# Optimization experiments

Hardware: AMD Instinct MI355X
Metric: run time of the kernel (lower is better)

The kernel has to match this reference:

```python
import jax, jax.numpy as jnp
import numpy as np

SEQ = 4096
D_MODEL = 2048


def setup_inputs() -> dict:
    key = jax.random.key(0)
    k1, k2, k3, k4 = jax.random.split(key, 4)
    scale = 1.0 / np.sqrt(D_MODEL)
    token_encodings = jax.random.normal(k1, (SEQ, D_MODEL), dtype=jnp.float32)
    W_q = jax.random.normal(k2, (D_MODEL, D_MODEL), dtype=jnp.float32) * scale
    W_k = jax.random.normal(k3, (D_MODEL, D_MODEL), dtype=jnp.float32) * scale
    W_v = jax.random.normal(k4, (D_MODEL, D_MODEL), dtype=jnp.float32) * scale
    # causal mask: True where attention is disallowed (strictly upper triangular),
    # mirroring `mask = mask == 0` applied to a lower-triangular ones matrix.
    mask = jnp.triu(jnp.ones((SEQ, SEQ), dtype=bool), k=1)
    return {"token_encodings": token_encodings, "W_q": W_q, "W_k": W_k,
            "W_v": W_v, "mask": mask}


def reference(token_encodings, W_q, W_k, W_v, mask):
    # nn.Linear(bias=False): y = x @ W.T
    q = token_encodings @ W_q.T  # [S, D]
    k = token_encodings @ W_k.T  # [S, D]
    v = token_encodings @ W_v.T  # [S, D]
    sims = q @ k.T               # [S, S]
    scaled = sims / jnp.asarray(np.sqrt(D_MODEL), dtype=sims.dtype)
    scaled = jnp.where(mask, jnp.asarray(-1e9, dtype=scaled.dtype), scaled)
    attn = jax.nn.softmax(scaled, axis=1)
    return attn @ v              # [S, D]
```

## Files before the change

### kernel.cpp

```cpp
#include <hip/hip_runtime.h>
#include <hip/hip_bf16.h>

typedef unsigned short u16;
typedef __attribute__((ext_vector_type(8))) short short8;
typedef __attribute__((ext_vector_type(4))) float f32x4;
typedef __attribute__((ext_vector_type(4))) unsigned short u16x4;

#define SEQL 4096
#define DMOD 2048

__device__ __forceinline__ u16 f2bf(float x) {
    unsigned int u = __float_as_uint(x);
    u += 0x7FFF + ((u >> 16) & 1);
    return (u16)(u >> 16);
}

__device__ __forceinline__ void async_copy16(const void* g, void* s) {
    __builtin_amdgcn_global_load_lds(
        (const __attribute__((address_space(1))) unsigned int*)g,
        (__attribute__((address_space(3))) unsigned int*)s,
        16, 0, 0);
}

__global__ __launch_bounds__(256)
void cast_all(const float* __restrict__ X,  const float* __restrict__ Wq,
              const float* __restrict__ Wk, const float* __restrict__ Wv,
              u16* __restrict__ Xb,  u16* __restrict__ Wqb,
              u16* __restrict__ Wkb, u16* __restrict__ Wvb)
{
    const int b = blockIdx.x;
    const float* in; u16* out; int i;
    if (b < 8192) { in = X; out = Xb; i = b * 256 + threadIdx.x; }
    else {
        const int w  = (b - 8192) >> 12;
        const int lb = (b - 8192) & 4095;
        i = lb * 256 + threadIdx.x;
        in  = w == 0 ? Wq  : w == 1 ? Wk  : Wv;
        out = w == 0 ? Wqb : w == 1 ? Wkb : Wvb;
    }
    float4 v = ((const float4*)in)[i];
    u16x4 r;
    r[0] = f2bf(v.x); r[1] = f2bf(v.y); r[2] = f2bf(v.z); r[3] = f2bf(v.w);
    ((u16x4*)out)[i] = r;
}

__global__ __launch_bounds__(256)
void gemm_qkv64(const u16* __restrict__ A,
                const u16* __restrict__ B0, const u16* __restrict__ B1, const u16* __restrict__ B2,
                u16* __restrict__ C0, u16* __restrict__ C1, u16* __restrict__ C2)
{
    const int K = DMOD, N = DMOD;
    const int bid = blockIdx.x;
    const int e = bid & 7, idx = bid >> 3;
    const int br = idx / 6;
    const int bcAll = e * 6 + idx % 6;
    const int which = bcAll >> 4;
    const int rowBase = br * 128, colBase = (bcAll & 15) * 128;
    const u16* B = which == 0 ? B0 : which == 1 ? B1 : B2;
    u16*       C = which == 0 ? C0 : which == 1 ? C1 : C2;

    __shared__ __align__(16) u16 As[2][128 * 64];
    __shared__ __align__(16) u16 Bs[2][128 * 64];

    const int tid = threadIdx.x;
    const int wid = tid >> 6, lane = tid & 63;
    const int wr = wid >> 1, wc = wid & 1;
    const int q = lane >> 4, l15 = lane & 15;

    const int nkt = K >> 6;
    const u16* Ag = A + (size_t)rowBase * K;
    const u16* Bg = B + (size_t)colBase * K;
    const int srow = lane >> 3;
    const int scel = ((lane & 7) * 8) ^ (srow << 3);

    f32x4 acc[4][4] = {};

    auto stage = [&](int buf, int kt) {
        const int k0 = kt * 64;
        #pragma unroll
        for (int r = 0; r < 4; ++r) {
            const int rowl = wid * 32 + r * 8;
            async_copy16(Ag + (size_t)(rowl + srow) * K + k0 + scel, &As[buf][rowl * 64]);
            async_copy16(Bg + (size_t)(rowl + srow) * K + k0 + scel, &Bs[buf][rowl * 64]);
        }
    };

    stage(0, 0);
    asm volatile("s_waitcnt vmcnt(0)" ::: "memory");
    __builtin_amdgcn_s_barrier();
    for (int kt = 0; kt < nkt; ++kt) {
        const int cur = kt & 1;
        if (kt + 1 < nkt) stage(cur ^ 1, kt + 1);

        short8 af[2][4], bfr[2][4];
        #pragma unroll
        for (int ks = 0; ks < 2; ++ks) {
            #pragma unroll
            for (int m = 0; m < 4; ++m) {
                const int row = wr * 64 + m * 16 + l15;
                af[ks][m] = *(const short8*)&As[cur][row * 64 + ((ks * 32 + q * 8) ^ ((row & 7) << 3))];
            }
            #pragma unroll
            for (int n = 0; n < 4; ++n) {
                const int row = wc * 64 + n * 16 + l15;
                bfr[ks][n] = *(const short8*)&Bs[cur][row * 64 + ((ks * 32 + q * 8) ^ ((row & 7) << 3))];
            }
        }
        #pragma unroll
        for (int ks = 0; ks < 2; ++ks)
            #pragma unroll
            for (int m = 0; m < 4; ++m)
                #pragma unroll
                for (int n = 0; n < 4; ++n)
                    acc[m][n] = __builtin_amdgcn_mfma_f32_16x16x32_bf16(
                        af[ks][m], bfr[ks][n], acc[m][n], 0, 0, 0);

        asm volatile("s_waitcnt vmcnt(0)" ::: "memory");
        __builtin_amdgcn_s_barrier();
    }

    const int crow0 = rowBase + wr * 64 + (lane >> 4) * 4;
    const int ccol0 = colBase + wc * 64 + l15;
    #pragma unroll
    for (int m = 0; m < 4; ++m)
        #pragma unroll
        for (int n = 0; n < 4; ++n)
            #pragma unroll
            for (int r = 0; r < 4; ++r)
                C[(size_t)(crow0 + m * 16 + r) * N + (ccol0 + n * 16)] = f2bf(acc[m][n][r]);
}

template<int MODE>
__global__ __launch_bounds__(256)
void gemm_bt64(const u16* __restrict__ A, const u16* __restrict__ B,
               void* __restrict__ Cout, float* __restrict__ lsum,
               int N, int K, float scale)
{
    int br, bc;
    if (MODE == 2) {
        const int bid = blockIdx.x;
        const int e = bid & 7, idx = bid >> 3;
        const int g = idx >> 1;
        br = (g < 16) ? (2 * g) : (63 - 2 * g);
        bc = e * 2 + (idx & 1);
    } else {
        br = blockIdx.y; bc = blockIdx.x;
        if (bc > br) return;
    }
    const int rowBase = br * 128, colBase = bc * 128;

    __shared__ __align__(16) u16 As[2][128 * 64];
    __shared__ __align__(16) u16 Bs[2][128 * 64];

    const int tid = threadIdx.x;
    const int wid = tid >> 6, lane = tid & 63;
    const int wr = wid >> 1, wc = wid & 1;
    const int q = lane >> 4, l15 = lane & 15;

    int nkt = K >> 6;
    if (MODE == 2) { const int lim = br * 2 + 2; if (lim < nkt) nkt = lim; }

    const u16* Ag = A + (size_t)rowBase * K;
    const u16* Bg = B + (size_t)colBase * K;
    const int srow = lane >> 3;
    const int scel = ((lane & 7) * 8) ^ (srow << 3);

    f32x4 acc[4][4] = {};

    auto stage = [&](int buf, int kt) {
        const int k0 = kt * 64;
        #pragma unroll
        for (int r = 0; r < 4; ++r) {
            const int rowl = wid * 32 + r * 8;
            async_copy16(Ag + (size_t)(rowl + srow) * K + k0 + scel, &As[buf][rowl * 64]);
            async_copy16(Bg + (size_t)(rowl + srow) * K + k0 + scel, &Bs[buf][rowl * 64]);
        }
    };

    stage(0, 0);
    asm volatile("s_waitcnt vmcnt(0)" ::: "memory");
    __builtin_amdgcn_s_barrier();
    for (int kt = 0; kt < nkt; ++kt) {
        const int cur = kt & 1;
        if (kt + 1 < nkt) stage(cur ^ 1, kt + 1);

        short8 af[2][4], bfr[2][4];
        #pragma unroll
        for (int ks = 0; ks < 2; ++ks) {
            #pragma unroll
            for (int m = 0; m < 4; ++m) {
                const int row = wr * 64 + m * 16 + l15;
                af[ks][m] = *(const short8*)&As[cur][row * 64 + ((ks * 32 + q * 8) ^ ((row & 7) << 3))];
            }
            #pragma unroll
            for (int n = 0; n < 4; ++n) {
                const int row = wc * 64 + n * 16 + l15;
                bfr[ks][n] = *(const short8*)&Bs[cur][row * 64 + ((ks * 32 + q * 8) ^ ((row & 7) << 3))];
            }
        }
        #pragma unroll
        for (int ks = 0; ks < 2; ++ks)
            #pragma unroll
            for (int m = 0; m < 4; ++m)
                #pragma unroll
                for (int n = 0; n < 4; ++n)
                    acc[m][n] = __builtin_amdgcn_mfma_f32_16x16x32_bf16(
                        af[ks][m], bfr[ks][n], acc[m][n], 0, 0, 0);

        asm volatile("s_waitcnt vmcnt(0)" ::: "memory");
        __builtin_amdgcn_s_barrier();
    }

    const int crow0 = rowBase + wr * 64 + (lane >> 4) * 4;
    const int ccol0 = colBase + wc * 64 + l15;
    if (MODE == 1) {
        u16* E = (u16*)Cout;
        #pragma unroll
        for (int m = 0; m < 4; ++m)
            #pragma unroll
            for (int r = 0; r < 4; ++r) {
                const int row = crow0 + m * 16 + r;
                float rs = 0.f;
                #pragma unroll
                for (int n = 0; n < 4; ++n) {
                    const int col = ccol0 + n * 16;
                    float e = (col > row) ? 0.f : __expf(acc[m][n][r] * scale);
                    E[(size_t)row * N + col] = f2bf(e);
                    rs += e;
                }
                rs += __shfl_xor(rs, 1);
                rs += __shfl_xor(rs, 2);
                rs += __shfl_xor(rs, 4);
                rs += __shfl_xor(rs, 8);
                if (l15 == 0) atomicAdd(&lsum[row], rs);
            }
    } else {
        float* C = (float*)Cout;
        #pragma unroll
        for (int m = 0; m < 4; ++m)
            #pragma unroll
            for (int r = 0; r < 4; ++r) {
                const int row = crow0 + m * 16 + r;
                const float inv = 1.0f / lsum[row];
                #pragma unroll
                for (int n = 0; n < 4; ++n)
                    C[(size_t)row * N + (ccol0 + n * 16)] = acc[m][n][r] * inv;
            }
    }
}

__global__ __launch_bounds__(256)
void transpose_bf16(const u16* __restrict__ in, u16* __restrict__ out, int R, int C) {
    __shared__ u16 t[64][65];
    const int cb = blockIdx.x * 64, rb = blockIdx.y * 64;
    const int tx = threadIdx.x & 63, ty = threadIdx.x >> 6;
    #pragma unroll
    for (int i = 0; i < 16; ++i) {
        const int r = i * 4 + ty;
        t[r][tx] = in[(size_t)(rb + r) * C + cb + tx];
    }
    __syncthreads();
    #pragma unroll
    for (int i = 0; i < 16; ++i) {
        const int r = i * 4 + ty;
        out[(size_t)(cb + r) * R + rb + tx] = t[tx][r];
    }
}

extern "C" void kernel_launch(void* const* d_in, const int* in_sizes, int n_in,
                              void* d_out, int out_size, void* d_ws, size_t ws_size,
                              hipStream_t stream)
{
    const float* X  = (const float*)d_in[0];
    const float* Wq = (const float*)d_in[1];
    const float* Wk = (const float*)d_in[2];
    const float* Wv = (const float*)d_in[3];
    float* Out = (float*)d_out;

    char* ws = (char*)d_ws;
    const size_t MB = 1ull << 20;
    u16*   Xb   = (u16*)(ws + 0);
    u16*   Wqb  = (u16*)(ws + 16 * MB);
    u16*   Wkb  = (u16*)(ws + 24 * MB);
    u16*   Wvb  = (u16*)(ws + 32 * MB);
    u16*   E    = (u16*)(ws + 16 * MB);
    u16*   Qb   = (u16*)(ws + 48 * MB);
    u16*   Kb   = (u16*)(ws + 64 * MB);
    u16*   Vb   = (u16*)(ws + 80 * MB);
    float* lsum = (float*)(ws + 96 * MB);

    const float scale = 0.022097086912079608f;

    hipMemsetAsync(lsum, 0, SEQL * sizeof(float), stream);

    cast_all<<<8192 + 3 * 4096, 256, 0, stream>>>(X, Wq, Wk, Wv, Xb, Wqb, Wkb, Wvb);

    gemm_qkv64<<<1536, 256, 0, stream>>>(Xb, Wqb, Wkb, Wvb, Qb, Kb, Vb);

    dim3 gS(SEQL / 128, SEQL / 128);
    gemm_bt64<1><<<gS, 256, 0, stream>>>(Qb, Kb, E, lsum, SEQL, DMOD, scale);

    u16* Vt = Xb;
    transpose_bf16<<<dim3(DMOD / 64, SEQL / 64), 256, 0, stream>>>(Vb, Vt, SEQL, DMOD);

    gemm_bt64<2><<<512, 256, 0, stream>>>(E, Vt, Out, lsum, DMOD, SEQL, 0.f);
}
```

Before: 292.0 us.

## Fuse V transpose into QKV GEMM epilogue and unroll k-loop by two

The V projection blocks now transpose their output tile through shared memory and write V^T directly, which removes the standalone transpose kernel and its extra read and write of V. Both GEMM kernels unroll the k-loop by two with constant buffer indices and precompute the per-lane load offset, cutting index arithmetic. Shared memory is merged into one array so the epilogue can reuse it for the transpose, at the cost of an extra barrier and LDS traffic in the V blocks. The unroll assumes an even tile count.

```diff
diff --git a/kernel.cpp b/kernel.cpp
--- a/kernel.cpp
+++ b/kernel.cpp
@@ -47,7 +47,7 @@
 __global__ __launch_bounds__(256)
 void gemm_qkv64(const u16* __restrict__ A,
                 const u16* __restrict__ B0, const u16* __restrict__ B1, const u16* __restrict__ B2,
-                u16* __restrict__ C0, u16* __restrict__ C1, u16* __restrict__ C2)
+                u16* __restrict__ C0, u16* __restrict__ C1, u16* __restrict__ Vt)
 {
     const int K = DMOD, N = DMOD;
     const int bid = blockIdx.x;
@@ -57,10 +57,10 @@
     const int which = bcAll >> 4;
     const int rowBase = br * 128, colBase = (bcAll & 15) * 128;
     const u16* B = which == 0 ? B0 : which == 1 ? B1 : B2;
-    u16*       C = which == 0 ? C0 : which == 1 ? C1 : C2;
-
-    __shared__ __align__(16) u16 As[2][128 * 64];
-    __shared__ __align__(16) u16 Bs[2][128 * 64];
+
+    __shared__ __align__(16) u16 sh[32768];
+    #define AS(buf, i) sh[(buf) * 8192 + (i)]
+    #define BS(buf, i) sh[16384 + (buf) * 8192 + (i)]
 
     const int tid = threadIdx.x;
     const int wid = tid >> 6, lane = tid & 63;
@@ -70,8 +70,7 @@
     const int nkt = K >> 6;
     const u16* Ag = A + (size_t)rowBase * K;
     const u16* Bg = B + (size_t)colBase * K;
-    const int srow = lane >> 3;
-    const int scel = ((lane & 7) * 8) ^ (srow << 3);
+    const int lofs = (lane >> 3) * K + (((lane & 7) * 8) ^ ((lane >> 3) << 3));
 
     f32x4 acc[4][4] = {};
 
@@ -80,54 +79,78 @@
         #pragma unroll
         for (int r = 0; r < 4; ++r) {
             const int rowl = wid * 32 + r * 8;
-            async_copy16(Ag + (size_t)(rowl + srow) * K + k0 + scel, &As[buf][rowl * 64]);
-            async_copy16(Bg + (size_t)(rowl + srow) * K + k0 + scel, &Bs[buf][rowl * 64]);
+            async_copy16(Ag + rowl * K + k0 + lofs, &AS(buf, rowl * 64));
+            async_copy16(Bg + rowl * K + k0 + lofs, &BS(buf, rowl * 64));
         }
     };
+
+#define TILE(CUR, KT)                                                              \
+    {                                                                              \
+        if ((KT) + 1 < nkt) stage((CUR) ^ 1, (KT) + 1);                            \
+        short8 af[2][4], bfr[2][4];                                                \
+        _Pragma("unroll") for (int ks = 0; ks < 2; ++ks) {                         \
+            _Pragma("unroll") for (int m = 0; m < 4; ++m) {                        \
+                const int row = wr * 64 + m * 16 + l15;                            \
+                af[ks][m] = *(const short8*)&AS(CUR,                               \
+                    row * 64 + ((ks * 32 + q * 8) ^ ((row & 7) << 3)));            \
+            }                                                                      \
+            _Pragma("unroll") for (int n = 0; n < 4; ++n) {                        \
+                const int row = wc * 64 + n * 16 + l15;                            \
+                bfr[ks][n] = *(const short8*)&BS(CUR,                              \
+                    row * 64 + ((ks * 32 + q * 8) ^ ((row & 7) << 3)));            \
+            }                                                                      \
+        }                                                                          \
+        _Pragma("unroll") for (int ks = 0; ks < 2; ++ks)                           \
+            _Pragma("unroll") for (int m = 0; m < 4; ++m)                          \
+                _Pragma("unroll") for (int n = 0; n < 4; ++n)                      \
+                    acc[m][n] = __builtin_amdgcn_mfma_f32_16x16x32_bf16(           \
+                        af[ks][m], bfr[ks][n], acc[m][n], 0, 0, 0);                \
+        asm volatile("s_waitcnt vmcnt(0)" ::: "memory");                           \
+        __builtin_amdgcn_s_barrier();                                              \
+    }
 
     stage(0, 0);
     asm volatile("s_waitcnt vmcnt(0)" ::: "memory");
     __builtin_amdgcn_s_barrier();
-    for (int kt = 0; kt < nkt; ++kt) {
-        const int cur = kt & 1;
-        if (kt + 1 < nkt) stage(cur ^ 1, kt + 1);
-
-        short8 af[2][4], bfr[2][4];
-        #pragma unroll
-        for (int ks = 0; ks < 2; ++ks) {
+    for (int kt = 0; kt < nkt; kt += 2) {
+        TILE(0, kt);
+        TILE(1, kt + 1);
+    }
+#undef TILE
+
+    if (which < 2) {
+        u16* C = which == 0 ? C0 : C1;
+        const int crow0 = rowBase + wr * 64 + (lane >> 4) * 4;
+        const int ccol0 = colBase + wc * 64 + l15;
+        #pragma unroll
+        for (int m = 0; m < 4; ++m)
             #pragma unroll
-            for (int m = 0; m < 4; ++m) {
-                const int row = wr * 64 + m * 16 + l15;
-                af[ks][m] = *(const short8*)&As[cur][row * 64 + ((ks * 32 + q * 8) ^ ((row & 7) << 3))];
-            }
+            for (int n = 0; n < 4; ++n)
+                #pragma unroll
+                for (int r = 0; r < 4; ++r)
+                    C[(size_t)(crow0 + m * 16 + r) * N + (ccol0 + n * 16)] = f2bf(acc[m][n][r]);
+    } else {
+        const int c0 = wc * 64 + l15;
+        const int r0 = wr * 64 + (lane >> 4) * 4;
+        #pragma unroll
+        for (int m = 0; m < 4; ++m)
             #pragma unroll
             for (int n = 0; n < 4; ++n) {
-                const int row = wc * 64 + n * 16 + l15;
-                bfr[ks][n] = *(const short8*)&Bs[cur][row * 64 + ((ks * 32 + q * 8) ^ ((row & 7) << 3))];
+                u16x4 p;
+                p[0] = f2bf(acc[m][n][0]); p[1] = f2bf(acc[m][n][1]);
+                p[2] = f2bf(acc[m][n][2]); p[3] = f2bf(acc[m][n][3]);
+                *(u16x4*)&sh[(c0 + n * 16) * 132 + r0 + m * 16] = p;
             }
-        }
-        #pragma unroll
-        for (int ks = 0; ks < 2; ++ks)
-            #pragma unroll
-            for (int m = 0; m < 4; ++m)
-                #pragma unroll
-                for (int n = 0; n < 4; ++n)
-                    acc[m][n] = __builtin_amdgcn_mfma_f32_16x16x32_bf16(
-                        af[ks][m], bfr[ks][n], acc[m][n], 0, 0, 0);
-
-        asm volatile("s_waitcnt vmcnt(0)" ::: "memory");
-        __builtin_amdgcn_s_barrier();
-    }
-
-    const int crow0 = rowBase + wr * 64 + (lane >> 4) * 4;
-    const int ccol0 = colBase + wc * 64 + l15;
-    #pragma unroll
-    for (int m = 0; m < 4; ++m)
-        #pragma unroll
-        for (int n = 0; n < 4; ++n)
-            #pragma unroll
-            for (int r = 0; r < 4; ++r)
-                C[(size_t)(crow0 + m * 16 + r) * N + (ccol0 + n * 16)] = f2bf(acc[m][n][r]);
+        __syncthreads();
+        const int vr = tid >> 1, h = tid & 1;
+        u16* dst = Vt + (size_t)(colBase + vr) * SEQL + rowBase + h * 64;
+        const u16* src = &sh[vr * 132 + h * 64];
+        #pragma unroll
+        for (int j = 0; j < 8; ++j)
+            *(short8*)&dst[j * 8] = *(const short8*)&src[j * 8];
+    }
+    #undef AS
+    #undef BS
 }
 
 template<int MODE>
@@ -162,8 +185,7 @@
 
     const u16* Ag = A + (size_t)rowBase * K;
     const u16* Bg = B + (size_t)colBase * K;
-    const int srow = lane >> 3;
-    const int scel = ((lane & 7) * 8) ^ (srow << 3);
+    const int lofs = (lane >> 3) * K + (((lane & 7) * 8) ^ ((lane >> 3) << 3));
 
     f32x4 acc[4][4] = {};
 
@@ -172,44 +194,44 @@
         #pragma unroll
         for (int r = 0; r < 4; ++r) {
             const int rowl = wid * 32 + r * 8;
-            async_copy16(Ag + (size_t)(rowl + srow) * K + k0 + scel, &As[buf][rowl * 64]);
-            async_copy16(Bg + (size_t)(rowl + srow) * K + k0 + scel, &Bs[buf][rowl * 64]);
+            async_copy16(Ag + rowl * K + k0 + lofs, &As[buf][rowl * 64]);
+            async_copy16(Bg + rowl * K + k0 + lofs, &Bs[buf][rowl * 64]);
         }
     };
+
+#define TILE(CUR, KT)                                                              \
+    {                                                                              \
+        if ((KT) + 1 < nkt) stage((CUR) ^ 1, (KT) + 1);                            \
+        short8 af[2][4], bfr[2][4];                                                \
+        _Pragma("unroll") for (int ks = 0; ks < 2; ++ks) {                         \
+            _Pragma("unroll") for (int m = 0; m < 4; ++m) {                        \
+                const int row = wr * 64 + m * 16 + l15;                            \
+                af[ks][m] = *(const short8*)&As[CUR][                              \
+                    row * 64 + ((ks * 32 + q * 8) ^ ((row & 7) << 3))];            \
+            }                                                                      \
+            _Pragma("unroll") for (int n = 0; n < 4; ++n) {                        \
+                const int row = wc * 64 + n * 16 + l15;                            \
+                bfr[ks][n] = *(const short8*)&Bs[CUR][                             \
+                    row * 64 + ((ks * 32 + q * 8) ^ ((row & 7) << 3))];            \
+            }                                                                      \
+        }                                                                          \
+        _Pragma("unroll") for (int ks = 0; ks < 2; ++ks)                           \
+            _Pragma("unroll") for (int m = 0; m < 4; ++m)                          \
+                _Pragma("unroll") for (int n = 0; n < 4; ++n)                      \
+                    acc[m][n] = __builtin_amdgcn_mfma_f32_16x16x32_bf16(           \
+                        af[ks][m], bfr[ks][n], acc[m][n], 0, 0, 0);                \
+        asm volatile("s_waitcnt vmcnt(0)" ::: "memory");                           \
+        __builtin_amdgcn_s_barrier();                                              \
+    }
 
     stage(0, 0);
     asm volatile("s_waitcnt vmcnt(0)" ::: "memory");
     __builtin_amdgcn_s_barrier();
-    for (int kt = 0; kt < nkt; ++kt) {
-        const int cur = kt & 1;
-        if (kt + 1 < nkt) stage(cur ^ 1, kt + 1);
-
-        short8 af[2][4], bfr[2][4];
-        #pragma unroll
-        for (int ks = 0; ks < 2; ++ks) {
-            #pragma unroll
-            for (int m = 0; m < 4; ++m) {
-                const int row = wr * 64 + m * 16 + l15;
-                af[ks][m] = *(const short8*)&As[cur][row * 64 + ((ks * 32 + q * 8) ^ ((row & 7) << 3))];
-            }
-            #pragma unroll
-            for (int n = 0; n < 4; ++n) {
-                const int row = wc * 64 + n * 16 + l15;
-                bfr[ks][n] = *(const short8*)&Bs[cur][row * 64 + ((ks * 32 + q * 8) ^ ((row & 7) << 3))];
-            }
-        }
-        #pragma unroll
-        for (int ks = 0; ks < 2; ++ks)
-            #pragma unroll
-            for (int m = 0; m < 4; ++m)
-                #pragma unroll
-                for (int n = 0; n < 4; ++n)
-                    acc[m][n] = __builtin_amdgcn_mfma_f32_16x16x32_bf16(
-                        af[ks][m], bfr[ks][n], acc[m][n], 0, 0, 0);
-
-        asm volatile("s_waitcnt vmcnt(0)" ::: "memory");
-        __builtin_amdgcn_s_barrier();
-    }
+    for (int kt = 0; kt < nkt; kt += 2) {
+        TILE(0, kt);
+        TILE(1, kt + 1);
+    }
+#undef TILE
 
     const int crow0 = rowBase + wr * 64 + (lane >> 4) * 4;
     const int ccol0 = colBase + wc * 64 + l15;
@@ -249,24 +271,6 @@
     }
 }
 
-__global__ __launch_bounds__(256)
-void transpose_bf16(const u16* __restrict__ in, u16* __restrict__ out, int R, int C) {
-    __shared__ u16 t[64][65];
-    const int cb = blockIdx.x * 64, rb = blockIdx.y * 64;
-    const int tx = threadIdx.x & 63, ty = threadIdx.x >> 6;
-    #pragma unroll
-    for (int i = 0; i < 16; ++i) {
-        const int r = i * 4 + ty;
-        t[r][tx] = in[(size_t)(rb + r) * C + cb + tx];
-    }
-    __syncthreads();
-    #pragma unroll
-    for (int i = 0; i < 16; ++i) {
-        const int r = i * 4 + ty;
-        out[(size_t)(cb + r) * R + rb + tx] = t[tx][r];
-    }
-}
-
 extern "C" void kernel_launch(void* const* d_in, const int* in_sizes, int n_in,
                               void* d_out, int out_size, void* d_ws, size_t ws_size,
                               hipStream_t stream)
@@ -286,7 +290,7 @@
     u16*   E    = (u16*)(ws + 16 * MB);
     u16*   Qb   = (u16*)(ws + 48 * MB);
     u16*   Kb   = (u16*)(ws + 64 * MB);
-    u16*   Vb   = (u16*)(ws + 80 * MB);
+    u16*   Vt   = (u16*)(ws + 80 * MB);
     float* lsum = (float*)(ws + 96 * MB);
 
     const float scale = 0.022097086912079608f;
@@ -295,13 +299,10 @@
 
     cast_all<<<8192 + 3 * 4096, 256, 0, stream>>>(X, Wq, Wk, Wv, Xb, Wqb, Wkb, Wvb);
 
-    gemm_qkv64<<<1536, 256, 0, stream>>>(Xb, Wqb, Wkb, Wvb, Qb, Kb, Vb);
+    gemm_qkv64<<<1536, 256, 0, stream>>>(Xb, Wqb, Wkb, Wvb, Qb, Kb, Vt);
 
     dim3 gS(SEQL / 128, SEQL / 128);
     gemm_bt64<1><<<gS, 256, 0, stream>>>(Qb, Kb, E, lsum, SEQL, DMOD, scale);
 
-    u16* Vt = Xb;
-    transpose_bf16<<<dim3(DMOD / 64, SEQL / 64), 256, 0, stream>>>(Vb, Vt, SEQL, DMOD);
-
     gemm_bt64<2><<<512, 256, 0, stream>>>(E, Vt, Out, lsum, DMOD, SEQL, 0.f);
 }
```

Measured after the change: 275.4 us. 5.7% less time.
